# Kernel optimization log

Hardware: AMD Instinct MI355X
Metric: run time of the kernel (lower is better)

The kernel has to match this reference:

```python
import jax, jax.numpy as jnp
import numpy as np

N, E, D, H, B = 10000, 160000, 128, 1, 4
SLOPE = 0.01  # negative_slope from DeepQNet default


def gat_layer(x, node_state, src, dst, W, att_src, att_dst, Wns, bns, bias):
    # x: [N,D] or [B,N,D]; node_state: [B,N,1]
    xs = x + node_state @ Wns + bns              # [B,N,D]
    Bx, Nn = xs.shape[0], xs.shape[1]
    h = (xs @ W).reshape(Bx, Nn, H, D)           # [B,N,H,C]
    a_src = (h * att_src).sum(-1)                # [B,N,H]
    a_dst = (h * att_dst).sum(-1)                # [B,N,H]
    ae = a_src[:, src] + a_dst[:, dst]           # [B,Etot,H]
    ae = jnp.where(ae > 0, ae, SLOPE * ae)       # leaky_relu
    ae_t = jnp.moveaxis(ae, 1, 0)                # [Etot,B,H]
    m = jax.ops.segment_max(ae_t, dst, num_segments=Nn)   # [N,B,H]
    e = jnp.exp(ae_t - m[dst])
    s = jax.ops.segment_sum(e, dst, num_segments=Nn)
    alpha = e / s[dst]                           # [Etot,B,H]
    h_e = jnp.moveaxis(h, 1, 0)                  # [N,B,H,C]
    msg = alpha[..., None] * h_e[src]            # [Etot,B,H,C]
    out = jax.ops.segment_sum(msg, dst, num_segments=Nn)  # [N,B,H,C]
    out = jnp.moveaxis(out, 0, 1).mean(2) + bias # concat=False -> head mean
    return jax.nn.relu(out)


def setup_inputs() -> dict:
    key = jax.random.key(0)
    ks = jax.random.split(key, 16)
    edges = jax.random.randint(ks[0], (2, E), 0, N)
    loop = jnp.arange(N)
    edge_index = jnp.concatenate([edges, jnp.stack([loop, loop])], axis=1)  # add_self_loops
    state = jax.random.uniform(ks[1], (B, N), dtype=jnp.float32)
    strucEmb = jax.random.normal(ks[2], (N, D), dtype=jnp.float32) * 0.1
    s = 0.05
    return {
        "state": state,
        "strucEmb": strucEmb,
        "edge_index": edge_index,
        "gat_W": jax.random.normal(ks[3], (3, D, H * D), dtype=jnp.float32) * s,
        "gat_att_src": jax.random.normal(ks[4], (3, H, D), dtype=jnp.float32) * s,
        "gat_att_dst": jax.random.normal(ks[5], (3, H, D), dtype=jnp.float32) * s,
        "gat_Wns": jax.random.normal(ks[6], (3, 1, D), dtype=jnp.float32) * s,
        "gat_bns": jnp.zeros((3, D), jnp.float32),
        "gat_bias": jnp.zeros((3, D), jnp.float32),
        "W1": jax.random.normal(ks[7], (D, D), dtype=jnp.float32) * s,
        "b1": jnp.zeros((D,), jnp.float32),
        "W2": jax.random.normal(ks[8], (D, D), dtype=jnp.float32) * s,
        "b2": jnp.zeros((D,), jnp.float32),
        "W3": jax.random.normal(ks[9], (2 * D, 1), dtype=jnp.float32) * s,
        "b3": jnp.zeros((1,), jnp.float32),
    }


def reference(state, strucEmb, edge_index, gat_W, gat_att_src, gat_att_dst,
              gat_Wns, gat_bns, gat_bias, W1, b1, W2, b2, W3, b3):
    src, dst = edge_index[0], edge_index[1]
    rs = state.reshape(state.shape[0], N, 1)     # [B,N,1]
    x = strucEmb
    for l in range(3):
        x = gat_layer(x, rs, src, dst, gat_W[l], gat_att_src[l], gat_att_dst[l],
                      gat_Wns[l], gat_bns[l], gat_bias[l])
    state_emb = x.sum(1)                         # [B,D]
    beta_state = state_emb @ W1 + b1             # [B,D]
    beta_action = x @ W2 + b2                    # [B,N,D]  (is_for_learn=True path)
    expand_state = jnp.broadcast_to(beta_state[:, None, :], beta_action.shape)
    out = jax.nn.relu(jnp.concatenate([expand_state, beta_action], axis=2))
    return out @ W3 + b3                         # [B,N,1]
```

## Files before the change

### kernel.cpp

```cpp
#include <hip/hip_runtime.h>
#include <math.h>

#define N_NODES 10000
#define B_SZ 4
#define SLOPE 0.01f
#define BN (B_SZ * N_NODES)
#define PADK 136

typedef __attribute__((ext_vector_type(8))) short short8;
typedef __attribute__((ext_vector_type(4))) float float4v;

__device__ __forceinline__ unsigned short f2bf(float f) {
    unsigned u = __builtin_bit_cast(unsigned, f);
    u += 0x7fffu + ((u >> 16) & 1u);
    return (unsigned short)(u >> 16);
}
__device__ __forceinline__ float bf2f(unsigned short s) {
    unsigned u = ((unsigned)s) << 16;
    return __builtin_bit_cast(float, u);
}
__device__ __forceinline__ float bflo(unsigned u) { return __builtin_bit_cast(float, u << 16); }
__device__ __forceinline__ float bfhi(unsigned u) { return __builtin_bit_cast(float, u & 0xffff0000u); }


__global__ __launch_bounds__(256) void setup_kernel(
    const float* __restrict__ strucEmb, const float* __restrict__ state,
    const float* __restrict__ Wns0, const float* __restrict__ bns0,
    const float* __restrict__ gatW, const float* __restrict__ W2,
    unsigned short* __restrict__ XS,
    unsigned short* __restrict__ whi, unsigned short* __restrict__ wlo,
    int* deg, int* cursor, float* state_emb)
{
    int bx = blockIdx.x, tid = threadIdx.x;
    if (bx < 20000) {
        int idx = bx * 256 + tid;
        int g = idx >> 7, d = idx & 127;
        int n = g >> 2, b = g & 3;
        float v = strucEmb[(size_t)n * 128 + d] + state[b * N_NODES + n] * Wns0[d] + bns0[d];
        XS[idx] = f2bf(v);
    } else if (bx < 20256) {
        int i = (bx - 20000) * 256 + tid;
        int w = i >> 14, rem = i & 16383;
        int k = rem >> 7, c = rem & 127;
        const float* src = (w < 3) ? (gatW + (size_t)w * 16384) : W2;
        float v = src[k * 128 + c];
        unsigned short h = f2bf(v);
        whi[w * 16384 + c * 128 + k] = h;
        wlo[w * 16384 + c * 128 + k] = f2bf(v - bf2f(h));
    } else {
        int i = (bx - 20256) * 256 + tid;
        if (i < N_NODES) { deg[i] = 0; cursor[i] = 0; }
        if (i < 512) state_emb[i] = 0.f;
    }
}


__global__ __launch_bounds__(256) void hist_kernel(const int* __restrict__ dst, int Etot, int* deg) {
    int e = blockIdx.x * 256 + threadIdx.x;
    if (e < Etot) atomicAdd(&deg[dst[e]], 1);
}

__global__ __launch_bounds__(1024) void scan_kernel(const int* __restrict__ deg, int* __restrict__ rowOff) {
    __shared__ int wsum[16];
    int tid = threadIdx.x;
    int lane = tid & 63, wid = tid >> 6;
    int base = tid * 10;
    int v[10]; int tot = 0;
#pragma unroll
    for (int j = 0; j < 10; j++) {
        int idx = base + j;
        int d = (idx < N_NODES) ? deg[idx] : 0;
        tot += d; v[j] = tot;
    }
    int incl = tot;
    for (int off = 1; off < 64; off <<= 1) {
        int t = __shfl_up(incl, off, 64);
        if (lane >= off) incl += t;
    }
    if (lane == 63) wsum[wid] = incl;
    __syncthreads();
    if (wid == 0) {
        int wv = (lane < 16) ? wsum[lane] : 0;
        for (int off = 1; off < 16; off <<= 1) {
            int t = __shfl_up(wv, off, 64);
            if (lane >= off) wv += t;
        }
        if (lane < 16) wsum[lane] = wv;
    }
    __syncthreads();
    int waveoff = (wid > 0) ? wsum[wid - 1] : 0;
    int excl = waveoff + incl - tot;
    if (tid == 0) rowOff[0] = 0;
#pragma unroll
    for (int j = 0; j < 10; j++) {
        int idx = base + j;
        if (idx < N_NODES) rowOff[idx + 1] = excl + v[j];
    }
}

__global__ __launch_bounds__(256) void scatter_kernel(const int* __restrict__ src, const int* __restrict__ dst,
                                                      int Etot, const int* __restrict__ rowOff,
                                                      int* cursor, int* __restrict__ srcLst) {
    int e = blockIdx.x * 256 + threadIdx.x;
    if (e < Etot) {
        int d = dst[e];
        int pos = rowOff[d] + atomicAdd(&cursor[d], 1);
        srcLst[pos] = src[e];
    }
}


__global__ __launch_bounds__(256) void gemm_att_mfma(
    const unsigned short* __restrict__ XS,
    const unsigned short* __restrict__ WThi, const unsigned short* __restrict__ WTlo,
    const float* __restrict__ attS, const float* __restrict__ attD,
    unsigned short* __restrict__ Hout, float* __restrict__ aSrcP, float* __restrict__ aDstP)
{
    __shared__ __align__(16) unsigned short sCus[64 * PADK];
    __shared__ float sAs[128], sAd[128];
    __shared__ float sPart[64 * 8];

    int tid = threadIdx.x;
    int g0 = blockIdx.x * 64;
    int w = tid >> 6, lane = tid & 63;
    int quad = lane >> 4, mcol = lane & 15;

    if (tid < 128) { sAs[tid] = attS[tid]; sAd[tid] = attD[tid]; }

    float4v acc[4][2];
#pragma unroll
    for (int mt = 0; mt < 4; mt++)
#pragma unroll
        for (int nt = 0; nt < 2; nt++) acc[mt][nt] = (float4v){0.f, 0.f, 0.f, 0.f};

#pragma unroll 1
    for (int term = 0; term < 2; term++) {
        const unsigned short* WT = term ? WTlo : WThi;
        short8 Bf[4][2];
#pragma unroll
        for (int kc = 0; kc < 4; kc++)
#pragma unroll
            for (int nt = 0; nt < 2; nt++)
                Bf[kc][nt] = *(const short8*)(WT + (w * 32 + nt * 16 + mcol) * 128 + kc * 32 + quad * 8);
#pragma unroll
        for (int kc = 0; kc < 4; kc++) {
            short8 Aa[4];
#pragma unroll
            for (int mt = 0; mt < 4; mt++)
                Aa[mt] = *(const short8*)(XS + (size_t)(g0 + mt * 16 + mcol) * 128 + kc * 32 + quad * 8);
#pragma unroll
            for (int mt = 0; mt < 4; mt++)
#pragma unroll
                for (int nt = 0; nt < 2; nt++)
                    acc[mt][nt] = __builtin_amdgcn_mfma_f32_16x16x32_bf16(Aa[mt], Bf[kc][nt], acc[mt][nt], 0, 0, 0);
        }
    }

    __syncthreads();

    float pp[16], pd[16];
#pragma unroll
    for (int r16 = 0; r16 < 16; r16++) { pp[r16] = 0.f; pd[r16] = 0.f; }
#pragma unroll
    for (int mt = 0; mt < 4; mt++)
#pragma unroll
        for (int nt = 0; nt < 2; nt++)
#pragma unroll
            for (int reg = 0; reg < 4; reg++) {
                int row = mt * 16 + quad * 4 + reg;
                int col = w * 32 + nt * 16 + mcol;
                float v = acc[mt][nt][reg];
                sCus[row * PADK + col] = f2bf(v);
                pp[mt * 4 + reg] += v * sAs[col];
                pd[mt * 4 + reg] += v * sAd[col];
            }
#pragma unroll
    for (int off = 1; off < 16; off <<= 1)
#pragma unroll
        for (int r16 = 0; r16 < 16; r16++) {
            pp[r16] += __shfl_xor(pp[r16], off);
            pd[r16] += __shfl_xor(pd[r16], off);
        }
    if (mcol == 0) {
#pragma unroll
        for (int r16 = 0; r16 < 16; r16++) {
            int row = (r16 >> 2) * 16 + quad * 4 + (r16 & 3);
            sPart[row * 8 + w * 2 + 0] = pp[r16];
            sPart[row * 8 + w * 2 + 1] = pd[r16];
        }
    }
    __syncthreads();

    for (int i = tid; i < 64 * 16; i += 256) {
        int r = i >> 4, c8 = i & 15;
        uint4 u = *(uint4*)(sCus + r * PADK + c8 * 8);
        *(uint4*)(Hout + (size_t)(g0 + r) * 128 + c8 * 8) = u;
    }
    if (tid < 64) {
        float s0 = sPart[tid * 8] + sPart[tid * 8 + 2] + sPart[tid * 8 + 4] + sPart[tid * 8 + 6];
        float s1 = sPart[tid * 8 + 1] + sPart[tid * 8 + 3] + sPart[tid * 8 + 5] + sPart[tid * 8 + 7];
        aSrcP[g0 + tid] = s0;
        aDstP[g0 + tid] = s1;
    }
}


__global__ __launch_bounds__(256) void sm_agg_kernel(
    const int* __restrict__ rowOff, const int* __restrict__ srcLst,
    const float* __restrict__ aSrcP, const float* __restrict__ aDstP,
    const unsigned short* __restrict__ H,
    const float* __restrict__ bias,
    const float* __restrict__ state, const float* __restrict__ wnsN,
    const float* __restrict__ bnsN, int addNext,
    unsigned short* __restrict__ Xout)
{
    __shared__ int   sSrcB[4 * 64];
    __shared__ float sAeB[4 * 64];
    int n = blockIdx.x;
    int start = rowOff[n], end = rowOff[n + 1];
    int cnt = end - start;
    int tid = threadIdx.x;
    int b = tid >> 6, t = tid & 63;
    float adst = aDstP[n * 4 + b];
    int*   sSrc = sSrcB + b * 64;
    float* sAe  = sAeB + b * 64;
    const uint4* H4 = (const uint4*)H;

    if (cnt <= 64) {
        float ae = -1e30f;
        if (t < cnt) {
            int sn = srcLst[start + t];
            sSrc[t] = sn;
            float v = aSrcP[sn * 4 + b] + adst;
            ae = v > 0.f ? v : SLOPE * v;
        }
        float m = ae;
        m = fmaxf(m, __shfl_xor(m, 1));  m = fmaxf(m, __shfl_xor(m, 2));
        m = fmaxf(m, __shfl_xor(m, 4));  m = fmaxf(m, __shfl_xor(m, 8));
        m = fmaxf(m, __shfl_xor(m, 16)); m = fmaxf(m, __shfl_xor(m, 32));
        float e = (t < cnt) ? __expf(ae - m) : 0.f;
        float s = e;
        s += __shfl_xor(s, 1);  s += __shfl_xor(s, 2);  s += __shfl_xor(s, 4);
        s += __shfl_xor(s, 8);  s += __shfl_xor(s, 16); s += __shfl_xor(s, 32);
        float inv = 1.f / s;
        if (t < cnt) sAe[t] = e * inv;
        int cntE = (cnt + 3) & ~3;
        if (t >= cnt && t < cntE) { sSrc[t] = n; sAe[t] = 0.f; }

        int esub = t >> 4, c16 = t & 15;
        float a0 = 0.f, a1 = 0.f, a2 = 0.f, a3 = 0.f, a4 = 0.f, a5 = 0.f, a6 = 0.f, a7 = 0.f;
        int j = 0;
        for (; j + 16 <= cntE; j += 16) {
            uint4 h[4]; float al[4];
#pragma unroll
            for (int r = 0; r < 4; r++) {
                int jj = j + r * 4 + esub;
                h[r] = H4[(size_t)(sSrc[jj] * 4 + b) * 16 + c16];
                al[r] = sAe[jj];
            }
#pragma unroll
            for (int r = 0; r < 4; r++) {
                a0 += al[r] * bflo(h[r].x); a1 += al[r] * bfhi(h[r].x);
                a2 += al[r] * bflo(h[r].y); a3 += al[r] * bfhi(h[r].y);
                a4 += al[r] * bflo(h[r].z); a5 += al[r] * bfhi(h[r].z);
                a6 += al[r] * bflo(h[r].w); a7 += al[r] * bfhi(h[r].w);
            }
        }
        for (; j < cntE; j += 4) {
            int jj = j + esub;
            uint4 hv = H4[(size_t)(sSrc[jj] * 4 + b) * 16 + c16];
            float al = sAe[jj];
            a0 += al * bflo(hv.x); a1 += al * bfhi(hv.x);
            a2 += al * bflo(hv.y); a3 += al * bfhi(hv.y);
            a4 += al * bflo(hv.z); a5 += al * bfhi(hv.z);
            a6 += al * bflo(hv.w); a7 += al * bfhi(hv.w);
        }
        a0 += __shfl_xor(a0, 16); a1 += __shfl_xor(a1, 16);
        a2 += __shfl_xor(a2, 16); a3 += __shfl_xor(a3, 16);
        a4 += __shfl_xor(a4, 16); a5 += __shfl_xor(a5, 16);
        a6 += __shfl_xor(a6, 16); a7 += __shfl_xor(a7, 16);
        a0 += __shfl_xor(a0, 32); a1 += __shfl_xor(a1, 32);
        a2 += __shfl_xor(a2, 32); a3 += __shfl_xor(a3, 32);
        a4 += __shfl_xor(a4, 32); a5 += __shfl_xor(a5, 32);
        a6 += __shfl_xor(a6, 32); a7 += __shfl_xor(a7, 32);
        if (esub == 0) {
            int d0 = c16 * 8;
            float o0 = fmaxf(a0 + bias[d0],     0.f);
            float o1 = fmaxf(a1 + bias[d0 + 1], 0.f);
            float o2 = fmaxf(a2 + bias[d0 + 2], 0.f);
            float o3 = fmaxf(a3 + bias[d0 + 3], 0.f);
            float o4 = fmaxf(a4 + bias[d0 + 4], 0.f);
            float o5 = fmaxf(a5 + bias[d0 + 5], 0.f);
            float o6 = fmaxf(a6 + bias[d0 + 6], 0.f);
            float o7 = fmaxf(a7 + bias[d0 + 7], 0.f);
            if (addNext) {
                float st = state[b * N_NODES + n];
                o0 += st * wnsN[d0]     + bnsN[d0];
                o1 += st * wnsN[d0 + 1] + bnsN[d0 + 1];
                o2 += st * wnsN[d0 + 2] + bnsN[d0 + 2];
                o3 += st * wnsN[d0 + 3] + bnsN[d0 + 3];
                o4 += st * wnsN[d0 + 4] + bnsN[d0 + 4];
                o5 += st * wnsN[d0 + 5] + bnsN[d0 + 5];
                o6 += st * wnsN[d0 + 6] + bnsN[d0 + 6];
                o7 += st * wnsN[d0 + 7] + bnsN[d0 + 7];
            }
            uint4 u;
            u.x = (unsigned)f2bf(o0) | ((unsigned)f2bf(o1) << 16);
            u.y = (unsigned)f2bf(o2) | ((unsigned)f2bf(o3) << 16);
            u.z = (unsigned)f2bf(o4) | ((unsigned)f2bf(o5) << 16);
            u.w = (unsigned)f2bf(o6) | ((unsigned)f2bf(o7) << 16);
            ((uint4*)Xout)[(size_t)(n * 4 + b) * 16 + c16] = u;
        }
    } else {
        const unsigned* Hu = (const unsigned*)H;
        float m = -1e30f;
        for (int i = start + t; i < end; i += 64) {
            int sn = srcLst[i];
            float v = aSrcP[sn * 4 + b] + adst;
            m = fmaxf(m, v > 0.f ? v : SLOPE * v);
        }
        m = fmaxf(m, __shfl_xor(m, 1));  m = fmaxf(m, __shfl_xor(m, 2));
        m = fmaxf(m, __shfl_xor(m, 4));  m = fmaxf(m, __shfl_xor(m, 8));
        m = fmaxf(m, __shfl_xor(m, 16)); m = fmaxf(m, __shfl_xor(m, 32));
        float s = 0.f;
        for (int i = start + t; i < end; i += 64) {
            int sn = srcLst[i];
            float v = aSrcP[sn * 4 + b] + adst;
            float ae2 = v > 0.f ? v : SLOPE * v;
            s += __expf(ae2 - m);
        }
        s += __shfl_xor(s, 1);  s += __shfl_xor(s, 2);  s += __shfl_xor(s, 4);
        s += __shfl_xor(s, 8);  s += __shfl_xor(s, 16); s += __shfl_xor(s, 32);
        float inv = 1.f / s;
        float accx = 0.f, accy = 0.f;
        for (int c0 = start; c0 < end; c0 += 64) {
            int c = min(64, end - c0);
            if (t < c) {
                int sn = srcLst[c0 + t];
                sSrc[t] = sn;
                float v = aSrcP[sn * 4 + b] + adst;
                float ae2 = v > 0.f ? v : SLOPE * v;
                sAe[t] = __expf(ae2 - m);
            }
            for (int j = 0; j < c; j++) {
                float a0 = sAe[j];
                unsigned h0 = Hu[(size_t)(sSrc[j] * 4 + b) * 64 + t];
                accx += a0 * bflo(h0);
                accy += a0 * bfhi(h0);
            }
        }
        float ox = fmaxf(accx * inv + bias[2 * t], 0.f);
        float oy = fmaxf(accy * inv + bias[2 * t + 1], 0.f);
        if (addNext) {
            float st = state[b * N_NODES + n];
            ox += st * wnsN[2 * t]     + bnsN[2 * t];
            oy += st * wnsN[2 * t + 1] + bnsN[2 * t + 1];
        }
        ((unsigned*)Xout)[(size_t)(n * 4 + b) * 64 + t] =
            (unsigned)f2bf(ox) | ((unsigned)f2bf(oy) << 16);
    }
}


__global__ __launch_bounds__(128) void sum_nodes_kernel(const unsigned short* __restrict__ X, float* state_emb) {
    int cx = blockIdx.x, b = blockIdx.y, d = threadIdx.x;
    int n0 = cx * 157, n1 = n0 + 157;
    if (n1 > N_NODES) n1 = N_NODES;
    float acc = 0.f;
    for (int n = n0; n < n1; n++) acc += bf2f(X[(size_t)(n * 4 + b) * 128 + d]);
    atomicAdd(&state_emb[b * 128 + d], acc);
}


__global__ __launch_bounds__(256) void final_mfma(
    const unsigned short* __restrict__ X,
    const unsigned short* __restrict__ WThi, const unsigned short* __restrict__ WTlo,
    const float* __restrict__ b2, const float* __restrict__ W3,
    const float* __restrict__ b3,
    const float* __restrict__ state_emb, const float* __restrict__ W1,
    const float* __restrict__ b1,
    float* __restrict__ out)
{
    __shared__ float sB2[128], sW3[128];
    __shared__ float sPart[64 * 4];
    __shared__ float sC1p[8], sC1[4];

    int tid = threadIdx.x;
    int g0 = blockIdx.x * 64;
    int w = tid >> 6, lane = tid & 63;
    int quad = lane >> 4, mcol = lane & 15;

    if (tid < 128) { sB2[tid] = b2[tid]; sW3[tid] = W3[128 + tid]; }

    {
        int d = tid & 127;
        int bh = tid >> 7;
        float p0 = b1[d], p1 = b1[d];
        for (int k = 0; k < 128; k++) {
            float wv = W1[k * 128 + d];
            p0 += state_emb[bh * 128 + k] * wv;
            p1 += state_emb[(bh + 2) * 128 + k] * wv;
        }
        float w3d = W3[d];
        p0 = fmaxf(p0, 0.f) * w3d;
        p1 = fmaxf(p1, 0.f) * w3d;
#pragma unroll
        for (int off = 1; off < 64; off <<= 1) {
            p0 += __shfl_xor(p0, off);
            p1 += __shfl_xor(p1, off);
        }
        if (lane == 0) { sC1p[w * 2 + 0] = p0; sC1p[w * 2 + 1] = p1; }
    }
    __syncthreads();
    if (tid == 0) {
        sC1[0] = sC1p[0] + sC1p[2];  sC1[2] = sC1p[1] + sC1p[3];
        sC1[1] = sC1p[4] + sC1p[6];  sC1[3] = sC1p[5] + sC1p[7];
    }

    float4v acc[4][2];
#pragma unroll
    for (int mt = 0; mt < 4; mt++)
#pragma unroll
        for (int nt = 0; nt < 2; nt++) acc[mt][nt] = (float4v){0.f, 0.f, 0.f, 0.f};

#pragma unroll 1
    for (int term = 0; term < 2; term++) {
        const unsigned short* WT = term ? WTlo : WThi;
        short8 Bf[4][2];
#pragma unroll
        for (int kc = 0; kc < 4; kc++)
#pragma unroll
            for (int nt = 0; nt < 2; nt++)
                Bf[kc][nt] = *(const short8*)(WT + (w * 32 + nt * 16 + mcol) * 128 + kc * 32 + quad * 8);
#pragma unroll
        for (int kc = 0; kc < 4; kc++) {
            short8 Aa[4];
#pragma unroll
            for (int mt = 0; mt < 4; mt++)
                Aa[mt] = *(const short8*)(X + (size_t)(g0 + mt * 16 + mcol) * 128 + kc * 32 + quad * 8);
#pragma unroll
            for (int mt = 0; mt < 4; mt++)
#pragma unroll
                for (int nt = 0; nt < 2; nt++)
                    acc[mt][nt] = __builtin_amdgcn_mfma_f32_16x16x32_bf16(Aa[mt], Bf[kc][nt], acc[mt][nt], 0, 0, 0);
        }
    }

    float pp[16];
#pragma unroll
    for (int r16 = 0; r16 < 16; r16++) pp[r16] = 0.f;
#pragma unroll
    for (int mt = 0; mt < 4; mt++)
#pragma unroll
        for (int nt = 0; nt < 2; nt++)
#pragma unroll
            for (int reg = 0; reg < 4; reg++) {
                int col = w * 32 + nt * 16 + mcol;
                float v = acc[mt][nt][reg] + sB2[col];
                v = v > 0.f ? v : 0.f;
                pp[mt * 4 + reg] += v * sW3[col];
            }
#pragma unroll
    for (int off = 1; off < 16; off <<= 1)
#pragma unroll
        for (int r16 = 0; r16 < 16; r16++)
            pp[r16] += __shfl_xor(pp[r16], off);
    if (mcol == 0) {
#pragma unroll
        for (int r16 = 0; r16 < 16; r16++) {
            int row = (r16 >> 2) * 16 + quad * 4 + (r16 & 3);
            sPart[row * 4 + w] = pp[r16];
        }
    }
    __syncthreads();
    if (tid < 64) {
        float p = sPart[tid * 4] + sPart[tid * 4 + 1] + sPart[tid * 4 + 2] + sPart[tid * 4 + 3];
        int g = g0 + tid;
        out[(g & 3) * N_NODES + (g >> 2)] = p + sC1[g & 3] + b3[0];
    }
}


extern "C" void kernel_launch(void* const* d_in, const int* in_sizes, int n_in,
                              void* d_out, int out_size, void* d_ws, size_t ws_size,
                              hipStream_t stream) {
    const float* state    = (const float*)d_in[0];
    const float* strucEmb = (const float*)d_in[1];
    const int*   edge_idx = (const int*)d_in[2];
    const float* gat_W    = (const float*)d_in[3];
    const float* gat_aS   = (const float*)d_in[4];
    const float* gat_aD   = (const float*)d_in[5];
    const float* gat_Wns  = (const float*)d_in[6];
    const float* gat_bns  = (const float*)d_in[7];
    const float* gat_bias = (const float*)d_in[8];
    const float* W1 = (const float*)d_in[9];
    const float* b1 = (const float*)d_in[10];
    const float* W2 = (const float*)d_in[11];
    const float* b2 = (const float*)d_in[12];
    const float* W3 = (const float*)d_in[13];
    const float* b3 = (const float*)d_in[14];
    float* out = (float*)d_out;

    int Etot = in_sizes[2] / 2;
    const int* srcArr = edge_idx;
    const int* dstArr = edge_idx + Etot;

    float* ws = (float*)d_ws;
    unsigned short* Xb = (unsigned short*)ws;
    unsigned short* Hb = (unsigned short*)(ws + 2560000);
    float* aSrcP       = ws + 5120000;
    float* aDstP       = ws + 5160000;
    float* state_emb   = ws + 5200000;
    unsigned short* whi = (unsigned short*)(ws + 5200516);
    unsigned short* wlo = whi + 4 * 16384;
    int*   iws         = (int*)(ws + 5200516 + 65536);
    int*   rowOff      = iws;
    int*   deg         = iws + 10001;
    int*   cursor      = deg + 10000;
    int*   srcLst      = cursor + 10000;

    setup_kernel<<<20296, 256, 0, stream>>>(strucEmb, state, gat_Wns, gat_bns,
                                            gat_W, W2, Xb, whi, wlo, deg, cursor, state_emb);
    hist_kernel<<<(Etot + 255) / 256, 256, 0, stream>>>(dstArr, Etot, deg);
    scan_kernel<<<1, 1024, 0, stream>>>(deg, rowOff);
    scatter_kernel<<<(Etot + 255) / 256, 256, 0, stream>>>(srcArr, dstArr, Etot, rowOff, cursor, srcLst);

    for (int l = 0; l < 3; l++) {
        gemm_att_mfma<<<BN / 64, 256, 0, stream>>>(
            Xb, whi + (size_t)l * 16384, wlo + (size_t)l * 16384,
            gat_aS + l * 128, gat_aD + l * 128, Hb, aSrcP, aDstP);
        sm_agg_kernel<<<N_NODES, 256, 0, stream>>>(
            rowOff, srcLst, aSrcP, aDstP, Hb, gat_bias + l * 128,
            state, gat_Wns + (l + 1 < 3 ? (l + 1) * 128 : 0),
            gat_bns + (l + 1 < 3 ? (l + 1) * 128 : 0), (l < 2) ? 1 : 0, Xb);
    }

    sum_nodes_kernel<<<dim3(64, B_SZ), 128, 0, stream>>>(Xb, state_emb);
    final_mfma<<<BN / 64, 256, 0, stream>>>(Xb, whi + 3 * 16384, wlo + 3 * 16384,
                                            b2, W3, b3, state_emb, W1, b1, out);
}
```

Measured before the change: 332.1 us.

## Switch activation layout to batch-major and map aggregation blocks to four nodes per batch

Node rows in the activation buffers move from node-major [N][B] interleaving to batch-major [B][N] order, and the setup, aggregation, node-sum and final kernels are reindexed to match. The aggregation grid becomes (N/4, B), so each block now handles four different nodes of one batch element instead of one node across four batches. The aim is better locality: the source-row gathers within a batch then hit a contiguous per-batch region, which may improve cache reuse. The trade-off is that the four wavefronts in a block no longer share the same edge list, and the parts of the code that were not shown, such as the GEMM's per-row batch index for sC1, must also agree with the new layout.

```diff
diff --git a/kernel.cpp b/kernel.cpp
--- a/kernel.cpp
+++ b/kernel.cpp
@@ -21,6 +21,7 @@
 }
 __device__ __forceinline__ float bflo(unsigned u) { return __builtin_bit_cast(float, u << 16); }
 __device__ __forceinline__ float bfhi(unsigned u) { return __builtin_bit_cast(float, u & 0xffff0000u); }
+
 
 
 __global__ __launch_bounds__(256) void setup_kernel(
@@ -35,8 +36,8 @@
     if (bx < 20000) {
         int idx = bx * 256 + tid;
         int g = idx >> 7, d = idx & 127;
-        int n = g >> 2, b = g & 3;
-        float v = strucEmb[(size_t)n * 128 + d] + state[b * N_NODES + n] * Wns0[d] + bns0[d];
+        int n = g - (g / N_NODES) * N_NODES;
+        float v = strucEmb[(size_t)n * 128 + d] + state[g] * Wns0[d] + bns0[d];
         XS[idx] = f2bf(v);
     } else if (bx < 20256) {
         int i = (bx - 20000) * 256 + tid;
@@ -216,14 +217,16 @@
 {
     __shared__ int   sSrcB[4 * 64];
     __shared__ float sAeB[4 * 64];
-    int n = blockIdx.x;
+    int tid = threadIdx.x;
+    int w = tid >> 6, t = tid & 63;
+    int n = blockIdx.x * 4 + w;
+    int b = blockIdx.y;
+    int gb = b * N_NODES;
     int start = rowOff[n], end = rowOff[n + 1];
     int cnt = end - start;
-    int tid = threadIdx.x;
-    int b = tid >> 6, t = tid & 63;
-    float adst = aDstP[n * 4 + b];
-    int*   sSrc = sSrcB + b * 64;
-    float* sAe  = sAeB + b * 64;
+    float adst = aDstP[gb + n];
+    int*   sSrc = sSrcB + w * 64;
+    float* sAe  = sAeB + w * 64;
     const uint4* H4 = (const uint4*)H;
 
     if (cnt <= 64) {
@@ -231,7 +234,7 @@
         if (t < cnt) {
             int sn = srcLst[start + t];
             sSrc[t] = sn;
-            float v = aSrcP[sn * 4 + b] + adst;
+            float v = aSrcP[gb + sn] + adst;
             ae = v > 0.f ? v : SLOPE * v;
         }
         float m = ae;
@@ -255,7 +258,7 @@
 #pragma unroll
             for (int r = 0; r < 4; r++) {
                 int jj = j + r * 4 + esub;
-                h[r] = H4[(size_t)(sSrc[jj] * 4 + b) * 16 + c16];
+                h[r] = H4[(size_t)(gb + sSrc[jj]) * 16 + c16];
                 al[r] = sAe[jj];
             }
 #pragma unroll
@@ -268,7 +271,7 @@
         }
         for (; j < cntE; j += 4) {
             int jj = j + esub;
-            uint4 hv = H4[(size_t)(sSrc[jj] * 4 + b) * 16 + c16];
+            uint4 hv = H4[(size_t)(gb + sSrc[jj]) * 16 + c16];
             float al = sAe[jj];
             a0 += al * bflo(hv.x); a1 += al * bfhi(hv.x);
             a2 += al * bflo(hv.y); a3 += al * bfhi(hv.y);
@@ -294,7 +297,7 @@
             float o6 = fmaxf(a6 + bias[d0 + 6], 0.f);
             float o7 = fmaxf(a7 + bias[d0 + 7], 0.f);
             if (addNext) {
-                float st = state[b * N_NODES + n];
+                float st = state[gb + n];
                 o0 += st * wnsN[d0]     + bnsN[d0];
                 o1 += st * wnsN[d0 + 1] + bnsN[d0 + 1];
                 o2 += st * wnsN[d0 + 2] + bnsN[d0 + 2];
@@ -309,14 +312,14 @@
             u.y = (unsigned)f2bf(o2) | ((unsigned)f2bf(o3) << 16);
             u.z = (unsigned)f2bf(o4) | ((unsigned)f2bf(o5) << 16);
             u.w = (unsigned)f2bf(o6) | ((unsigned)f2bf(o7) << 16);
-            ((uint4*)Xout)[(size_t)(n * 4 + b) * 16 + c16] = u;
+            ((uint4*)Xout)[(size_t)(gb + n) * 16 + c16] = u;
         }
     } else {
         const unsigned* Hu = (const unsigned*)H;
         float m = -1e30f;
         for (int i = start + t; i < end; i += 64) {
             int sn = srcLst[i];
-            float v = aSrcP[sn * 4 + b] + adst;
+            float v = aSrcP[gb + sn] + adst;
             m = fmaxf(m, v > 0.f ? v : SLOPE * v);
         }
         m = fmaxf(m, __shfl_xor(m, 1));  m = fmaxf(m, __shfl_xor(m, 2));
@@ -325,7 +328,7 @@
         float s = 0.f;
         for (int i = start + t; i < end; i += 64) {
             int sn = srcLst[i];
-            float v = aSrcP[sn * 4 + b] + adst;
+            float v = aSrcP[gb + sn] + adst;
             float ae2 = v > 0.f ? v : SLOPE * v;
             s += __expf(ae2 - m);
         }
@@ -338,13 +341,13 @@
             if (t < c) {
                 int sn = srcLst[c0 + t];
                 sSrc[t] = sn;
-                float v = aSrcP[sn * 4 + b] + adst;
+                float v = aSrcP[gb + sn] + adst;
                 float ae2 = v > 0.f ? v : SLOPE * v;
                 sAe[t] = __expf(ae2 - m);
             }
             for (int j = 0; j < c; j++) {
                 float a0 = sAe[j];
-                unsigned h0 = Hu[(size_t)(sSrc[j] * 4 + b) * 64 + t];
+                unsigned h0 = Hu[(size_t)(gb + sSrc[j]) * 64 + t];
                 accx += a0 * bflo(h0);
                 accy += a0 * bfhi(h0);
             }
@@ -352,11 +355,11 @@
         float ox = fmaxf(accx * inv + bias[2 * t], 0.f);
         float oy = fmaxf(accy * inv + bias[2 * t + 1], 0.f);
         if (addNext) {
-            float st = state[b * N_NODES + n];
+            float st = state[gb + n];
             ox += st * wnsN[2 * t]     + bnsN[2 * t];
             oy += st * wnsN[2 * t + 1] + bnsN[2 * t + 1];
         }
-        ((unsigned*)Xout)[(size_t)(n * 4 + b) * 64 + t] =
+        ((unsigned*)Xout)[(size_t)(gb + n) * 64 + t] =
             (unsigned)f2bf(ox) | ((unsigned)f2bf(oy) << 16);
     }
 }
@@ -367,7 +370,7 @@
     int n0 = cx * 157, n1 = n0 + 157;
     if (n1 > N_NODES) n1 = N_NODES;
     float acc = 0.f;
-    for (int n = n0; n < n1; n++) acc += bf2f(X[(size_t)(n * 4 + b) * 128 + d]);
+    for (int n = n0; n < n1; n++) acc += bf2f(X[(size_t)(b * N_NODES + n) * 128 + d]);
     atomicAdd(&state_emb[b * 128 + d], acc);
 }
 
@@ -476,7 +479,8 @@
     if (tid < 64) {
         float p = sPart[tid * 4] + sPart[tid * 4 + 1] + sPart[tid * 4 + 2] + sPart[tid * 4 + 3];
         int g = g0 + tid;
-        out[(g & 3) * N_NODES + (g >> 2)] = p + sC1[g & 3] + b3[0];
+        int b = g / N_NODES;
+        out[g] = p + sC1[b] + b3[0];
     }
 }
 
@@ -529,7 +533,7 @@
         gemm_att_mfma<<<BN / 64, 256, 0, stream>>>(
             Xb, whi + (size_t)l * 16384, wlo + (size_t)l * 16384,
             gat_aS + l * 128, gat_aD + l * 128, Hb, aSrcP, aDstP);
-        sm_agg_kernel<<<N_NODES, 256, 0, stream>>>(
+        sm_agg_kernel<<<dim3(N_NODES / 4, B_SZ), 256, 0, stream>>>(
             rowOff, srcLst, aSrcP, aDstP, Hb, gat_bias + l * 128,
             state, gat_Wns + (l + 1 < 3 ? (l + 1) * 128 : 0),
             gat_bns + (l + 1 < 3 ? (l + 1) * 128 : 0), (l < 2) ? 1 : 0, Xb);
```

After: 328.3 us. About the same (-1.1%).
